# Optimization experiments

Hardware: AMD Instinct MI355X
Metric: run time of the kernel (lower is better)

The kernel has to match this reference:

```python
import jax, jax.numpy as jnp
import numpy as np

B, L, D, H, DH, MAX_SEQ = 2, 2048, 512, 8, 64, 2048


def setup_inputs() -> dict:
    key = jax.random.key(0)
    ks = jax.random.split(key, 9)
    w = 0.02
    return {
        "q": jax.random.normal(ks[0], (B, L, D), jnp.float32),
        "k": jax.random.normal(ks[1], (B, L, D), jnp.float32),
        "v": jax.random.normal(ks[2], (B, L, D), jnp.float32),
        "Wq_w": jax.random.normal(ks[3], (D, D), jnp.float32) * w,
        "Wq_b": jnp.zeros((D,), jnp.float32),
        "Wk_w": jax.random.normal(ks[4], (D, D), jnp.float32) * w,
        "Wk_b": jnp.zeros((D,), jnp.float32),
        "Wv_w": jax.random.normal(ks[5], (D, D), jnp.float32) * w,
        "Wv_b": jnp.zeros((D,), jnp.float32),
        "fc_w": jax.random.normal(ks[6], (D, D), jnp.float32) * w,
        "fc_b": jnp.zeros((D,), jnp.float32),
        "E": jax.random.normal(ks[7], (MAX_SEQ, DH), jnp.float32),
        "mask": jnp.triu(jnp.ones((L, L), jnp.int32), k=1)[None, None],  # 1 = masked
    }


def reference(q, k, v, Wq_w, Wq_b, Wk_w, Wk_b, Wv_w, Wv_b, fc_w, fc_b, E, mask):
    b, lq, d = q.shape

    def proj(x, w, bias):
        # torch Linear: x @ W.T + b, then split heads -> [b, h, l, dh]
        y = x @ w.T + bias
        return y.reshape(b, -1, H, DH).transpose(0, 2, 1, 3)

    qh, kh, vh = proj(q, Wq_w, Wq_b), proj(k, Wk_w, Wk_b), proj(v, Wv_w, Wv_b)
    len_q, len_k = qh.shape[2], kh.shape[2]

    # relative embedding slice (starting_point = max(0, max_seq - len_q))
    e = E[max(0, MAX_SEQ - len_q):, :]          # [m, dh], m == len_q here
    m = e.shape[0]

    QE = jnp.einsum('bhld,md->bhlm', qh, e)      # [b,h,lq,m]
    # qe_masking: keep column j of row i iff j >= m-1-i
    keep = (jnp.arange(m)[None, :] >= (m - 1 - jnp.arange(len_q))[:, None])
    QE = QE * keep.astype(QE.dtype)

    # skewing: left-pad last dim, reshape swapping trailing dims, drop first row
    padded = jnp.pad(QE, ((0, 0), (0, 0), (0, 0), (1, 0)))      # [b,h,lq,m+1]
    Srel = padded.reshape(b, H, m + 1, len_q)[:, :, 1:, :]       # [b,h,m,lq]
    if len_k > len_q:
        Srel = jnp.pad(Srel, ((0, 0), (0, 0), (0, len_k - len_q), (0, 0)))
    elif len_k < len_q:
        Srel = Srel[:, :, :, :len_k]

    QKt = jnp.einsum('bhld,bhmd->bhlm', qh, kh)                  # [b,h,lq,lk]
    logits = (QKt + Srel) / jnp.sqrt(jnp.float32(DH))
    logits = logits + mask.astype(logits.dtype) * jnp.float32(-1e9)
    attn = jax.nn.softmax(logits, axis=-1)
    out = jnp.einsum('bhlm,bhmd->bhld', attn, vh)                # [b,h,lq,dh]
    out = out.transpose(0, 2, 1, 3).reshape(b, len_q, d)
    out = out @ fc_w.T + fc_b
    return out, attn
```

## Files before the change

### kernel.cpp

```cpp
#include <hip/hip_runtime.h>
#include <hip/hip_bf16.h>
#include <cstdint>

typedef __bf16 bf16;
typedef __attribute__((ext_vector_type(8))) __bf16 bf16x8;
typedef __attribute__((ext_vector_type(4))) __bf16 bf16x4;
typedef __attribute__((ext_vector_type(4))) float f32x4;

#define MFMA16 __builtin_amdgcn_mfma_f32_16x16x32_bf16
#define MASKV (-1e30f)

static constexpr int Lq  = 2048;
static constexpr int BQ  = 64;
static constexpr int BKt = 64;
static constexpr int TW  = 84;

__device__ __forceinline__ void async_load16(const void* g, void* l) {
  __builtin_amdgcn_global_load_lds(
      (__attribute__((address_space(1))) void*)g,
      (__attribute__((address_space(3))) void*)l, 16, 0, 0);
}

__global__ void convert_all(const float* __restrict__ q, const float* __restrict__ k,
                            const float* __restrict__ v, const float* __restrict__ wq,
                            const float* __restrict__ wk, const float* __restrict__ wv,
                            const float* __restrict__ fc, const float* __restrict__ E,
                            bf16* q_bf, bf16* k_bf, bf16* v_bf, bf16* wq_bf,
                            bf16* wk_bf, bf16* wv_bf, bf16* fc_bf, bf16* E_bf)
{
  int i = blockIdx.x * blockDim.x + threadIdx.x;
  const float* src; bf16* dst; int rel;
  if      (i < 524288)  { src = q;  dst = q_bf;  rel = i; }
  else if (i < 1048576) { src = k;  dst = k_bf;  rel = i - 524288; }
  else if (i < 1572864) { src = v;  dst = v_bf;  rel = i - 1048576; }
  else if (i < 1638400) { src = wq; dst = wq_bf; rel = i - 1572864; }
  else if (i < 1703936) { src = wk; dst = wk_bf; rel = i - 1638400; }
  else if (i < 1769472) { src = wv; dst = wv_bf; rel = i - 1703936; }
  else if (i < 1835008) { src = fc; dst = fc_bf; rel = i - 1769472; }
  else if (i < 1867776) { src = E;  dst = E_bf;  rel = i - 1835008; }
  else return;
  float4 x = *(const float4*)(src + (size_t)rel * 4);
  bf16x4 o;
  o[0] = (bf16)x.x; o[1] = (bf16)x.y; o[2] = (bf16)x.z; o[3] = (bf16)x.w;
  *(bf16x4*)(dst + (size_t)rel * 4) = o;
}

template<int MODE>
__global__ __launch_bounds__(256, 2)
void gemm512(const bf16* __restrict__ A, const bf16* __restrict__ Bm,
             const float* __restrict__ bias, void* __restrict__ Cv)
{
  __shared__ __align__(16) char lA[16384];
  __shared__ __align__(16) char lB[16384];
  const int tid = threadIdx.x, lane = tid & 63, wv = tid >> 6;
  const int wr = wv >> 1, wc = wv & 1;
  const int tm = blockIdx.x, tn = blockIdx.y;

  f32x4 acc[4][4];
#pragma unroll
  for (int m = 0; m < 4; ++m)
#pragma unroll
    for (int n = 0; n < 4; ++n) acc[m][n] = (f32x4){0.f, 0.f, 0.f, 0.f};

  for (int k0 = 0; k0 < 512; k0 += 64) {
    __syncthreads();
#pragma unroll
    for (int it = 0; it < 4; ++it) {
      int slot = it * 256 + wv * 64 + lane;
      int row = slot >> 3, c = slot & 7;
      int gk = k0 + ((c ^ (row & 7)) * 8);
      async_load16(A  + (size_t)(tm * 128 + row) * 512 + gk, lA + (it * 256 + wv * 64) * 16);
      async_load16(Bm + (size_t)(tn * 128 + row) * 512 + gk, lB + (it * 256 + wv * 64) * 16);
    }
    __syncthreads();
#pragma unroll
    for (int kc = 0; kc < 2; ++kc) {
      bf16x8 af[4], bfr[4];
#pragma unroll
      for (int m = 0; m < 4; ++m) {
        int row = wr * 64 + m * 16 + (lane & 15);
        int ch = ((lane >> 4) + kc * 4) ^ (row & 7);
        af[m] = *(const bf16x8*)(lA + row * 128 + ch * 16);
      }
#pragma unroll
      for (int n = 0; n < 4; ++n) {
        int row = wc * 64 + n * 16 + (lane & 15);
        int ch = ((lane >> 4) + kc * 4) ^ (row & 7);
        bfr[n] = *(const bf16x8*)(lB + row * 128 + ch * 16);
      }
#pragma unroll
      for (int m = 0; m < 4; ++m)
#pragma unroll
        for (int n = 0; n < 4; ++n)
          acc[m][n] = MFMA16(af[m], bfr[n], acc[m][n], 0, 0, 0);
    }
  }

#pragma unroll
  for (int m = 0; m < 4; ++m)
#pragma unroll
    for (int n = 0; n < 4; ++n)
#pragma unroll
      for (int r = 0; r < 4; ++r) {
        int gi = tm * 128 + wr * 64 + m * 16 + 4 * (lane >> 4) + r;
        int gj = tn * 128 + wc * 64 + n * 16 + (lane & 15);
        float vv = acc[m][n][r] + ((MODE == 2) ? bias[gi] : bias[gj]);
        if (MODE == 3) {
          ((float*)Cv)[(size_t)gi * 512 + gj] = vv;
        } else if (MODE == 2) {
          int h = gi >> 6, dh = gi & 63, b = gj >> 11, l = gj & 2047;
          ((bf16*)Cv)[((size_t)((b * 8 + h) * 64 + dh)) * 2048 + l] = (bf16)vv;
        } else {
          int b = gi >> 11, l = gi & 2047, h = gj >> 6, dh = gj & 63;
          ((bf16*)Cv)[((size_t)((b * 8 + h) * 2048 + l)) * 64 + dh] = (bf16)vv;
        }
      }
}

__device__ __forceinline__ void stage_k(const bf16* __restrict__ kb, int j0,
                                        char* dst, int tid) {
#pragma unroll
  for (int it = 0; it < 2; ++it) {
    int slot = it * 256 + tid;
    int row = slot >> 3, c = slot & 7;
    async_load16(kb + (size_t)(j0 + row) * 64 + ((c ^ (row & 7)) * 8), dst + slot * 16);
  }
}
__device__ __forceinline__ void stage_v(const bf16* __restrict__ vb, int j0,
                                        char* dst, int tid) {
#pragma unroll
  for (int it = 0; it < 2; ++it) {
    int slot = it * 256 + tid;
    int row = slot >> 3, c = slot & 7;
    async_load16(vb + (size_t)row * Lq + j0 + ((c ^ (row & 7)) * 8), dst + slot * 16);
  }
}

__device__ __forceinline__ void attn_logits3(
    int i0, int j0, int wvx, int lane,
    const bf16x8 qf0, const bf16x8 qf1,
    const bf16* __restrict__ Ebf, const char* lk, bf16* tst, f32x4 acc_s[4])
{
  const int rbase = i0 + wvx * 16 - j0 - 63;
  f32x4 acc_t[5];
#pragma unroll
  for (int cf = 0; cf < 5; ++cf) {
    int r = rbase + cf * 16 + (lane & 15);
    int re = 2047 - r; re = re < 0 ? 0 : (re > 2047 ? 2047 : re);
    const bf16* ep = Ebf + (size_t)re * 64 + (lane >> 4) * 8;
    f32x4 a = (f32x4){0.f, 0.f, 0.f, 0.f};
    a = MFMA16(qf0, *(const bf16x8*)ep, a, 0, 0, 0);
    a = MFMA16(qf1, *(const bf16x8*)(ep + 32), a, 0, 0, 0);
    acc_t[cf] = a;
  }
#pragma unroll
  for (int cf = 0; cf < 4; ++cf) {
    int key = cf * 16 + (lane & 15);
    int c0 = (lane >> 4) ^ (key & 7);
    int c1 = ((lane >> 4) + 4) ^ (key & 7);
    f32x4 a = (f32x4){0.f, 0.f, 0.f, 0.f};
    a = MFMA16(qf0, *(const bf16x8*)(lk + key * 128 + c0 * 16), a, 0, 0, 0);
    a = MFMA16(qf1, *(const bf16x8*)(lk + key * 128 + c1 * 16), a, 0, 0, 0);
    acc_s[cf] = a;
  }
#pragma unroll
  for (int cf = 0; cf < 5; ++cf)
#pragma unroll
    for (int r = 0; r < 4; ++r)
      tst[(4 * (lane >> 4) + r) * TW + cf * 16 + (lane & 15)] = (bf16)acc_t[cf][r];
  asm volatile("s_waitcnt lgkmcnt(0)" ::: "memory");
  __builtin_amdgcn_sched_barrier(0);
#pragma unroll
  for (int cf = 0; cf < 4; ++cf) {
    int kl = cf * 16 + (lane & 15);
#pragma unroll
    for (int r = 0; r < 4; ++r) {
      int qw = 4 * (lane >> 4) + r;
      float t = (float)tst[qw * TW + (qw - kl + 63)];
      float vv = (acc_s[cf][r] + t) * 0.125f;
      if (j0 + kl > i0 + wvx * 16 + qw) vv = MASKV;
      acc_s[cf][r] = vv;
    }
  }
}

__global__ __launch_bounds__(256, 2)
void attn_kernel(const bf16* __restrict__ qh, const bf16* __restrict__ kh,
                 const bf16* __restrict__ vt, const bf16* __restrict__ Ebf,
                 float* __restrict__ attn_out, bf16* __restrict__ oh)
{
  __shared__ __align__(16) char lds_k[2][64 * 128];
  __shared__ __align__(16) char lds_v[2][64 * 128];
  __shared__ __align__(16) char lds_t[4][16 * TW * 2];

  const int tid = threadIdx.x, lane = tid & 63, wvx = tid >> 6;
  const int n    = blockIdx.x;
  const int half = n >> 8;
  const int r0   = n & 255;
  const int xcd  = r0 & 7;
  const int idx  = r0 >> 3;
  const int bh   = 2 * xcd + half;
  const int qt   = half ? idx : 31 - idx;
  const int i0   = qt * BQ;

  const bf16* qb = qh + (size_t)bh * Lq * 64;
  const bf16* kb = kh + (size_t)bh * Lq * 64;
  const bf16* vb = vt + (size_t)bh * 64 * Lq;
  float* attn_b = attn_out + (size_t)bh * Lq * Lq;
  bf16* tst = (bf16*)lds_t[wvx];
  bf16* pst = tst;

  const int qrow = i0 + wvx * 16 + (lane & 15);
  const bf16x8 qf0 = *(const bf16x8*)(qb + (size_t)qrow * 64 + (lane >> 4) * 8);
  const bf16x8 qf1 = *(const bf16x8*)(qb + (size_t)qrow * 64 + 32 + (lane >> 4) * 8);

  f32x4 acc_s[4];
  f32x4 acc_o[4];
  float s_acc[4] = {0.f, 0.f, 0.f, 0.f};
#pragma unroll
  for (int nn = 0; nn < 4; ++nn) acc_o[nn] = (f32x4){0.f, 0.f, 0.f, 0.f};

  stage_k(kb, 0, lds_k[0], tid);
  stage_v(vb, 0, lds_v[0], tid);
  __syncthreads();
  for (int jt = 0; jt <= qt; ++jt) {
    const int j0 = jt * BKt;
    if (jt < qt) {
      stage_k(kb, j0 + BKt, lds_k[(jt + 1) & 1], tid);
      stage_v(vb, j0 + BKt, lds_v[(jt + 1) & 1], tid);
    }
    attn_logits3(i0, j0, wvx, lane, qf0, qf1, Ebf, lds_k[jt & 1], tst, acc_s);
    asm volatile("" ::: "memory");
#pragma unroll
    for (int cf = 0; cf < 4; ++cf) {
      int kl = cf * 16 + (lane & 15);
      int chs = kl >> 3;
#pragma unroll
      for (int r = 0; r < 4; ++r) {
        int qw = 4 * (lane >> 4) + r;
        float p = __expf(acc_s[cf][r]);
        s_acc[r] += p;
        pst[qw * 64 + ((chs ^ (qw & 7)) * 8) + (kl & 7)] = (bf16)p;
      }
    }
    asm volatile("s_waitcnt lgkmcnt(0)" ::: "memory");
    __builtin_amdgcn_sched_barrier(0);
#pragma unroll
    for (int it = 0; it < 2; ++it) {
      int qw = it * 8 + (lane >> 3);
      int c = lane & 7;
      bf16x8 pv = *(const bf16x8*)(pst + qw * 64 + ((c ^ (qw & 7)) * 8));
      float* dst = attn_b + (size_t)(i0 + wvx * 16 + qw) * Lq + j0 + c * 8;
      float4 f0, f1;
      f0.x = (float)pv[0]; f0.y = (float)pv[1]; f0.z = (float)pv[2]; f0.w = (float)pv[3];
      f1.x = (float)pv[4]; f1.y = (float)pv[5]; f1.z = (float)pv[6]; f1.w = (float)pv[7];
      *(float4*)dst = f0; *(float4*)(dst + 4) = f1;
    }
#pragma unroll
    for (int kc = 0; kc < 2; ++kc) {
      int qa = lane & 15;
      int cha = (kc * 4 + (lane >> 4)) ^ (qa & 7);
      bf16x8 pf = *(const bf16x8*)(pst + qa * 64 + cha * 8);
#pragma unroll
      for (int nn = 0; nn < 4; ++nn) {
        int dh = nn * 16 + (lane & 15);
        int chv = (kc * 4 + (lane >> 4)) ^ (dh & 7);
        bf16x8 vf = *(const bf16x8*)(lds_v[jt & 1] + dh * 128 + chv * 16);
        acc_o[nn] = MFMA16(pf, vf, acc_o[nn], 0, 0, 0);
      }
    }
    __syncthreads();
  }

  float inv_s[4];
#pragma unroll
  for (int r = 0; r < 4; ++r) {
    float s = s_acc[r];
    for (int d = 1; d < 16; d <<= 1) s += __shfl_xor(s, d);
    inv_s[r] = 1.f / s;
  }

  const int b = bh >> 3, h = bh & 7;
#pragma unroll
  for (int nn = 0; nn < 4; ++nn)
#pragma unroll
    for (int r = 0; r < 4; ++r) {
      int qw = 4 * (lane >> 4) + r;
      int ig = i0 + wvx * 16 + qw;
      int col = h * 64 + nn * 16 + (lane & 15);
      oh[(size_t)(b * 2048 + ig) * 512 + col] = (bf16)(acc_o[nn][r] * inv_s[r]);
    }

  asm volatile("s_waitcnt vmcnt(0)" ::: "memory");
  const int ncols = (qt + 1) * BKt;
  const int jlane = (lane & 15) * 4;
  for (int j = jlane; j < ncols; j += 64) {
#pragma unroll
    for (int r = 0; r < 4; ++r) {
      float* p = attn_b + (size_t)(i0 + wvx * 16 + 4 * (lane >> 4) + r) * Lq + j;
      float4 x = *(float4*)p;
      x.x *= inv_s[r]; x.y *= inv_s[r]; x.z *= inv_s[r]; x.w *= inv_s[r];
      *(float4*)p = x;
    }
  }
  for (int j = ncols + jlane; j < Lq; j += 64) {
#pragma unroll
    for (int r = 0; r < 4; ++r) {
      float* p = attn_b + (size_t)(i0 + wvx * 16 + 4 * (lane >> 4) + r) * Lq + j;
      *(float4*)p = make_float4(0.f, 0.f, 0.f, 0.f);
    }
  }
}

extern "C" void kernel_launch(void* const* d_in, const int* in_sizes, int n_in,
                              void* d_out, int out_size, void* d_ws, size_t ws_size,
                              hipStream_t stream) {
  const float* q    = (const float*)d_in[0];
  const float* k    = (const float*)d_in[1];
  const float* v    = (const float*)d_in[2];
  const float* wq   = (const float*)d_in[3];
  const float* wq_b = (const float*)d_in[4];
  const float* wk   = (const float*)d_in[5];
  const float* wk_b = (const float*)d_in[6];
  const float* wv   = (const float*)d_in[7];
  const float* wv_b = (const float*)d_in[8];
  const float* fc   = (const float*)d_in[9];
  const float* fc_b = (const float*)d_in[10];
  const float* E    = (const float*)d_in[11];

  if (ws_size < 31719424) return;
  char* ws = (char*)d_ws;
  bf16* q_bf  = (bf16*)(ws);
  bf16* k_bf  = (bf16*)(ws + 4194304);
  bf16* v_bf  = (bf16*)(ws + 8388608);
  bf16* wq_bf = (bf16*)(ws + 12582912);
  bf16* wk_bf = (bf16*)(ws + 13107200);
  bf16* wv_bf = (bf16*)(ws + 13631488);
  bf16* fc_bf = (bf16*)(ws + 14155776);
  bf16* E_bf  = (bf16*)(ws + 14680064);
  bf16* qh_bf = (bf16*)(ws + 14942208);
  bf16* kh_bf = (bf16*)(ws + 19136512);
  bf16* vt_bf = (bf16*)(ws + 23330816);
  bf16* oh_bf = (bf16*)(ws + 27525120);

  float* out_f  = (float*)d_out;
  float* attn_f = out_f + 2097152;

  convert_all<<<7296, 256, 0, stream>>>(q, k, v, wq, wk, wv, fc, E,
      q_bf, k_bf, v_bf, wq_bf, wk_bf, wv_bf, fc_bf, E_bf);
  gemm512<0><<<dim3(32, 4), 256, 0, stream>>>(q_bf, wq_bf, wq_b, qh_bf);
  gemm512<0><<<dim3(32, 4), 256, 0, stream>>>(k_bf, wk_bf, wk_b, kh_bf);
  gemm512<2><<<dim3(4, 32), 256, 0, stream>>>(wv_bf, v_bf, wv_b, vt_bf);
  attn_kernel<<<512, 256, 0, stream>>>(qh_bf, kh_bf, vt_bf, E_bf, attn_f, oh_bf);
  gemm512<3><<<dim3(32, 4), 256, 0, stream>>>(oh_bf, fc_bf, fc_b, out_f);
}
```

Baseline: 222.1 us.

## Split attention into row-sum pass and KV-split main pass with combine

Adds a first pass that computes the softmax denominators (split over key-tile chunks, reduced with atomics), so the main attention kernel can write normalized probabilities directly instead of re-reading and rescaling the attention matrix. The main kernel is also split into two halves over key tiles, producing partial outputs that a separate kernel sums. This removes the read-modify-write pass over the large attention output and increases parallelism. In exchange, the logits are computed twice, and the extra launches and the partial-output round trip add cost.

After: 213.0 us. 4.1% less time.

```diff
diff --git a/kernel.cpp b/kernel.cpp
--- a/kernel.cpp
+++ b/kernel.cpp
@@ -45,6 +45,23 @@
   *(bf16x4*)(dst + (size_t)rel * 4) = o;
 }
 
+__global__ void zero_s(float* __restrict__ s_buf) {
+  int i = blockIdx.x * blockDim.x + threadIdx.x;
+  if (i < 8192) ((float4*)s_buf)[i] = make_float4(0.f, 0.f, 0.f, 0.f);
+}
+
+__global__ void combine_o(const bf16* __restrict__ O0, const bf16* __restrict__ O1,
+                          bf16* __restrict__ oh) {
+  int i = blockIdx.x * blockDim.x + threadIdx.x;
+  if (i >= 262144) return;
+  bf16x8 a = *(const bf16x8*)(O0 + (size_t)i * 8);
+  bf16x8 b = *(const bf16x8*)(O1 + (size_t)i * 8);
+  bf16x8 o;
+#pragma unroll
+  for (int j = 0; j < 8; ++j) o[j] = (bf16)((float)a[j] + (float)b[j]);
+  *(bf16x8*)(oh + (size_t)i * 8) = o;
+}
+
 template<int MODE>
 __global__ __launch_bounds__(256, 2)
 void gemm512(const bf16* __restrict__ A, const bf16* __restrict__ Bm,
@@ -184,24 +201,83 @@
   }
 }
 
-__global__ __launch_bounds__(256, 2)
-void attn_kernel(const bf16* __restrict__ qh, const bf16* __restrict__ kh,
-                 const bf16* __restrict__ vt, const bf16* __restrict__ Ebf,
-                 float* __restrict__ attn_out, bf16* __restrict__ oh)
+__global__ __launch_bounds__(256, 4)
+void pass1_sums(const bf16* __restrict__ qh, const bf16* __restrict__ kh,
+                const bf16* __restrict__ Ebf, float* __restrict__ s_buf)
+{
+  __shared__ __align__(16) char lds_k[2][64 * 128];
+  __shared__ __align__(16) char lds_t[4][16 * TW * 2];
+  const int tid = threadIdx.x, lane = tid & 63, wvx = tid >> 6;
+  const int bid = blockIdx.x;
+  const int bh  = bid / 144;
+  int f = bid - bh * 144, qt = 0;
+#pragma unroll 1
+  for (int q = 0; q < 32; ++q) {
+    int c = (q + 4) >> 2;
+    if (f < c) { qt = q; break; }
+    f -= c;
+  }
+  const int jbeg = f * 4;
+  const int jend = (jbeg + 4 < qt + 1) ? jbeg + 4 : qt + 1;
+  const int i0 = qt * BQ;
+
+  const bf16* qb = qh + (size_t)bh * Lq * 64;
+  const bf16* kb = kh + (size_t)bh * Lq * 64;
+  bf16* tst = (bf16*)lds_t[wvx];
+
+  const int qrow = i0 + wvx * 16 + (lane & 15);
+  const bf16x8 qf0 = *(const bf16x8*)(qb + (size_t)qrow * 64 + (lane >> 4) * 8);
+  const bf16x8 qf1 = *(const bf16x8*)(qb + (size_t)qrow * 64 + 32 + (lane >> 4) * 8);
+
+  f32x4 acc_s[4];
+  float s_acc[4] = {0.f, 0.f, 0.f, 0.f};
+
+  stage_k(kb, jbeg * BKt, lds_k[0], tid);
+  __syncthreads();
+  for (int jt = jbeg; jt < jend; ++jt) {
+    const int lt = (jt - jbeg) & 1;
+    if (jt + 1 < jend) stage_k(kb, (jt + 1) * BKt, lds_k[lt ^ 1], tid);
+    attn_logits3(i0, jt * BKt, wvx, lane, qf0, qf1, Ebf, lds_k[lt], tst, acc_s);
+#pragma unroll
+    for (int r = 0; r < 4; ++r) {
+#pragma unroll
+      for (int cf = 0; cf < 4; ++cf) s_acc[r] += __expf(acc_s[cf][r]);
+    }
+    __syncthreads();
+  }
+#pragma unroll
+  for (int r = 0; r < 4; ++r) {
+    float s = s_acc[r];
+    for (int d = 1; d < 16; d <<= 1) s += __shfl_xor(s, d);
+    if ((lane & 15) == 0)
+      atomicAdd(&s_buf[bh * Lq + i0 + wvx * 16 + 4 * (lane >> 4) + r], s);
+  }
+}
+
+__global__ __launch_bounds__(256, 3)
+void attn_main(const bf16* __restrict__ qh, const bf16* __restrict__ kh,
+               const bf16* __restrict__ vt, const bf16* __restrict__ Ebf,
+               const float* __restrict__ s_buf, float* __restrict__ attn_out,
+               bf16* __restrict__ O0, bf16* __restrict__ O1)
 {
   __shared__ __align__(16) char lds_k[2][64 * 128];
   __shared__ __align__(16) char lds_v[2][64 * 128];
   __shared__ __align__(16) char lds_t[4][16 * TW * 2];
 
   const int tid = threadIdx.x, lane = tid & 63, wvx = tid >> 6;
-  const int n    = blockIdx.x;
-  const int half = n >> 8;
-  const int r0   = n & 255;
+  const int x    = blockIdx.x, jh = blockIdx.y;
+  const int half = x >> 8;
+  const int r0   = x & 255;
   const int xcd  = r0 & 7;
   const int idx  = r0 >> 3;
   const int bh   = 2 * xcd + half;
   const int qt   = half ? idx : 31 - idx;
   const int i0   = qt * BQ;
+  const int njt  = qt + 1;
+  const int nj0  = (njt + 1) >> 1;
+  const int jbeg = jh ? nj0 : 0;
+  const int jend = jh ? njt : nj0;
+  bf16* Opart = jh ? O1 : O0;
 
   const bf16* qb = qh + (size_t)bh * Lq * 64;
   const bf16* kb = kh + (size_t)bh * Lq * 64;
@@ -214,70 +290,68 @@
   const bf16x8 qf0 = *(const bf16x8*)(qb + (size_t)qrow * 64 + (lane >> 4) * 8);
   const bf16x8 qf1 = *(const bf16x8*)(qb + (size_t)qrow * 64 + 32 + (lane >> 4) * 8);
 
+  float inv_s[4];
+#pragma unroll
+  for (int r = 0; r < 4; ++r)
+    inv_s[r] = 1.f / s_buf[bh * Lq + i0 + wvx * 16 + 4 * (lane >> 4) + r];
+
   f32x4 acc_s[4];
   f32x4 acc_o[4];
-  float s_acc[4] = {0.f, 0.f, 0.f, 0.f};
 #pragma unroll
   for (int nn = 0; nn < 4; ++nn) acc_o[nn] = (f32x4){0.f, 0.f, 0.f, 0.f};
 
-  stage_k(kb, 0, lds_k[0], tid);
-  stage_v(vb, 0, lds_v[0], tid);
-  __syncthreads();
-  for (int jt = 0; jt <= qt; ++jt) {
-    const int j0 = jt * BKt;
-    if (jt < qt) {
-      stage_k(kb, j0 + BKt, lds_k[(jt + 1) & 1], tid);
-      stage_v(vb, j0 + BKt, lds_v[(jt + 1) & 1], tid);
-    }
-    attn_logits3(i0, j0, wvx, lane, qf0, qf1, Ebf, lds_k[jt & 1], tst, acc_s);
-    asm volatile("" ::: "memory");
-#pragma unroll
-    for (int cf = 0; cf < 4; ++cf) {
-      int kl = cf * 16 + (lane & 15);
-      int chs = kl >> 3;
-#pragma unroll
-      for (int r = 0; r < 4; ++r) {
-        int qw = 4 * (lane >> 4) + r;
-        float p = __expf(acc_s[cf][r]);
-        s_acc[r] += p;
-        pst[qw * 64 + ((chs ^ (qw & 7)) * 8) + (kl & 7)] = (bf16)p;
-      }
-    }
-    asm volatile("s_waitcnt lgkmcnt(0)" ::: "memory");
-    __builtin_amdgcn_sched_barrier(0);
-#pragma unroll
-    for (int it = 0; it < 2; ++it) {
-      int qw = it * 8 + (lane >> 3);
-      int c = lane & 7;
-      bf16x8 pv = *(const bf16x8*)(pst + qw * 64 + ((c ^ (qw & 7)) * 8));
-      float* dst = attn_b + (size_t)(i0 + wvx * 16 + qw) * Lq + j0 + c * 8;
-      float4 f0, f1;
-      f0.x = (float)pv[0]; f0.y = (float)pv[1]; f0.z = (float)pv[2]; f0.w = (float)pv[3];
-      f1.x = (float)pv[4]; f1.y = (float)pv[5]; f1.z = (float)pv[6]; f1.w = (float)pv[7];
-      *(float4*)dst = f0; *(float4*)(dst + 4) = f1;
-    }
-#pragma unroll
-    for (int kc = 0; kc < 2; ++kc) {
-      int qa = lane & 15;
-      int cha = (kc * 4 + (lane >> 4)) ^ (qa & 7);
-      bf16x8 pf = *(const bf16x8*)(pst + qa * 64 + cha * 8);
-#pragma unroll
-      for (int nn = 0; nn < 4; ++nn) {
-        int dh = nn * 16 + (lane & 15);
-        int chv = (kc * 4 + (lane >> 4)) ^ (dh & 7);
-        bf16x8 vf = *(const bf16x8*)(lds_v[jt & 1] + dh * 128 + chv * 16);
-        acc_o[nn] = MFMA16(pf, vf, acc_o[nn], 0, 0, 0);
-      }
-    }
+  if (jbeg < jend) {
+    stage_k(kb, jbeg * BKt, lds_k[0], tid);
+    stage_v(vb, jbeg * BKt, lds_v[0], tid);
     __syncthreads();
-  }
-
-  float inv_s[4];
-#pragma unroll
-  for (int r = 0; r < 4; ++r) {
-    float s = s_acc[r];
-    for (int d = 1; d < 16; d <<= 1) s += __shfl_xor(s, d);
-    inv_s[r] = 1.f / s;
+    for (int jt = jbeg; jt < jend; ++jt) {
+      const int j0 = jt * BKt;
+      const int lt = (jt - jbeg) & 1;
+      if (jt + 1 < jend) {
+        stage_k(kb, j0 + BKt, lds_k[lt ^ 1], tid);
+        stage_v(vb, j0 + BKt, lds_v[lt ^ 1], tid);
+      }
+      attn_logits3(i0, j0, wvx, lane, qf0, qf1, Ebf, lds_k[lt], tst, acc_s);
+      asm volatile("" ::: "memory");
+#pragma unroll
+      for (int cf = 0; cf < 4; ++cf) {
+        int kl = cf * 16 + (lane & 15);
+        int chs = kl >> 3;
+#pragma unroll
+        for (int r = 0; r < 4; ++r) {
+          int qw = 4 * (lane >> 4) + r;
+          float p = __expf(acc_s[cf][r]) * inv_s[r];
+          pst[qw * 64 + ((chs ^ (qw & 7)) * 8) + (kl & 7)] = (bf16)p;
+        }
+      }
+      asm volatile("s_waitcnt lgkmcnt(0)" ::: "memory");
+      __builtin_amdgcn_sched_barrier(0);
+#pragma unroll
+      for (int it = 0; it < 2; ++it) {
+        int qw = it * 8 + (lane >> 3);
+        int c = lane & 7;
+        bf16x8 pv = *(const bf16x8*)(pst + qw * 64 + ((c ^ (qw & 7)) * 8));
+        float* dst = attn_b + (size_t)(i0 + wvx * 16 + qw) * Lq + j0 + c * 8;
+        float4 f0, f1;
+        f0.x = (float)pv[0]; f0.y = (float)pv[1]; f0.z = (float)pv[2]; f0.w = (float)pv[3];
+        f1.x = (float)pv[4]; f1.y = (float)pv[5]; f1.z = (float)pv[6]; f1.w = (float)pv[7];
+        *(float4*)dst = f0; *(float4*)(dst + 4) = f1;
+      }
+#pragma unroll
+      for (int kc = 0; kc < 2; ++kc) {
+        int qa = lane & 15;
+        int cha = (kc * 4 + (lane >> 4)) ^ (qa & 7);
+        bf16x8 pf = *(const bf16x8*)(pst + qa * 64 + cha * 8);
+#pragma unroll
+        for (int nn = 0; nn < 4; ++nn) {
+          int dh = nn * 16 + (lane & 15);
+          int chv = (kc * 4 + (lane >> 4)) ^ (dh & 7);
+          bf16x8 vf = *(const bf16x8*)(lds_v[lt] + dh * 128 + chv * 16);
+          acc_o[nn] = MFMA16(pf, vf, acc_o[nn], 0, 0, 0);
+        }
+      }
+      __syncthreads();
+    }
   }
 
   const int b = bh >> 3, h = bh & 7;
@@ -288,26 +362,17 @@
       int qw = 4 * (lane >> 4) + r;
       int ig = i0 + wvx * 16 + qw;
       int col = h * 64 + nn * 16 + (lane & 15);
-      oh[(size_t)(b * 2048 + ig) * 512 + col] = (bf16)(acc_o[nn][r] * inv_s[r]);
-    }
-
-  asm volatile("s_waitcnt vmcnt(0)" ::: "memory");
-  const int ncols = (qt + 1) * BKt;
-  const int jlane = (lane & 15) * 4;
-  for (int j = jlane; j < ncols; j += 64) {
-#pragma unroll
-    for (int r = 0; r < 4; ++r) {
-      float* p = attn_b + (size_t)(i0 + wvx * 16 + 4 * (lane >> 4) + r) * Lq + j;
-      float4 x = *(float4*)p;
-      x.x *= inv_s[r]; x.y *= inv_s[r]; x.z *= inv_s[r]; x.w *= inv_s[r];
-      *(float4*)p = x;
-    }
-  }
-  for (int j = ncols + jlane; j < Lq; j += 64) {
-#pragma unroll
-    for (int r = 0; r < 4; ++r) {
-      float* p = attn_b + (size_t)(i0 + wvx * 16 + 4 * (lane >> 4) + r) * Lq + j;
-      *(float4*)p = make_float4(0.f, 0.f, 0.f, 0.f);
+      Opart[(size_t)(b * 2048 + ig) * 512 + col] = (bf16)acc_o[nn][r];
+    }
+
+  if (jh == 1) {
+    const int jlane = (lane & 15) * 4;
+    for (int j = njt * BKt + jlane; j < Lq; j += 64) {
+#pragma unroll
+      for (int r = 0; r < 4; ++r) {
+        float* p = attn_b + (size_t)(i0 + wvx * 16 + 4 * (lane >> 4) + r) * Lq + j;
+        *(float4*)p = make_float4(0.f, 0.f, 0.f, 0.f);
+      }
     }
   }
 }
@@ -343,14 +408,22 @@
   bf16* vt_bf = (bf16*)(ws + 23330816);
   bf16* oh_bf = (bf16*)(ws + 27525120);
 
+  bf16*  O0    = (bf16*)(ws);
+  bf16*  O1    = (bf16*)(ws + 4194304);
+  float* s_buf = (float*)(ws + 12582912);
+
   float* out_f  = (float*)d_out;
   float* attn_f = out_f + 2097152;
 
   convert_all<<<7296, 256, 0, stream>>>(q, k, v, wq, wk, wv, fc, E,
       q_bf, k_bf, v_bf, wq_bf, wk_bf, wv_bf, fc_bf, E_bf);
   gemm512<0><<<dim3(32, 4), 256, 0, stream>>>(q_bf, wq_bf, wq_b, qh_bf);
+  zero_s<<<32, 256, 0, stream>>>(s_buf);
   gemm512<0><<<dim3(32, 4), 256, 0, stream>>>(k_bf, wk_bf, wk_b, kh_bf);
   gemm512<2><<<dim3(4, 32), 256, 0, stream>>>(wv_bf, v_bf, wv_b, vt_bf);
-  attn_kernel<<<512, 256, 0, stream>>>(qh_bf, kh_bf, vt_bf, E_bf, attn_f, oh_bf);
+  pass1_sums<<<2304, 256, 0, stream>>>(qh_bf, kh_bf, E_bf, s_buf);
+  attn_main<<<dim3(512, 2), 256, 0, stream>>>(qh_bf, kh_bf, vt_bf, E_bf,
+                                              s_buf, attn_f, O0, O1);
+  combine_o<<<1024, 256, 0, stream>>>(O0, O1, oh_bf);
   gemm512<3><<<dim3(32, 4), 256, 0, stream>>>(oh_bf, fc_bf, fc_b, out_f);
 }
```
